# Kernel optimization log

Hardware: AMD Instinct MI355X
Metric: run time of the kernel (lower is better)

Reference implementation:

```python
import jax, jax.numpy as jnp
import numpy as np

B, S, N, P = 16, 1, 6, 70000
H0, W0, DS = 448, 800, 4
H, W = H0 // DS, W0 // DS          # 112, 200
BEV_SIDE = 200


def _apply_4x4(RT, xyz):
    # RT: [M,4,4], xyz: [M,P,3] -> [M,P,3]
    xyz1 = jnp.concatenate([xyz, jnp.ones_like(xyz[..., :1])], axis=-1)
    return jnp.einsum('mij,mpj->mpi', RT, xyz1)[..., :3]


def _scale_intrinsics4(K, sx, sy):
    # K: [M,3,3] pinhole intrinsics -> scaled, embedded in 4x4
    M = K.shape[0]
    K4 = jnp.tile(jnp.eye(4, dtype=K.dtype), (M, 1, 1))
    K4 = K4.at[:, 0, 0].set(K[:, 0, 0] * sx)
    K4 = K4.at[:, 1, 1].set(K[:, 1, 1] * sy)
    K4 = K4.at[:, 0, 2].set(K[:, 0, 2] * sx)
    K4 = K4.at[:, 1, 2].set(K[:, 1, 2] * sy)
    return K4


def setup_inputs() -> dict:
    rng = np.random.default_rng(0)
    pts = rng.uniform(-50.0, 50.0, size=(B, 1, 1, P, 3)).astype(np.float32)
    pts[..., 2] = rng.uniform(-2.0, 4.0, size=(B, 1, 1, P)).astype(np.float32)
    ilu = rng.uniform(0.0, 255.0, size=(B, 1, 1, P, 1)).astype(np.float32)
    pcloud = np.concatenate([pts, ilu], axis=-1)
    # extrinsics: cam-to-car pose, 6 cameras at yaw 0..300deg
    E = np.tile(np.eye(4, dtype=np.float32), (B, S, N, 1, 1))
    for n in range(N):
        a = 2.0 * np.pi * n / N
        c, s = np.cos(a), np.sin(a)
        E[:, :, n, :3, :3] = np.array([[c, -s, 0], [s, c, 0], [0, 0, 1]], np.float32)
        E[:, :, n, :3, 3] = np.array([2.0 * c, 2.0 * s, 1.5], np.float32)
    K = np.tile(np.eye(3, dtype=np.float32), (B, S, N, 1, 1))
    K[..., 0, 0] = 500.0
    K[..., 1, 1] = 500.0
    K[..., 0, 2] = W0 / 2.0
    K[..., 1, 2] = H0 / 2.0
    V = np.tile(np.eye(4, dtype=np.float32), (B, 1, 1, 1, 1))
    V[..., 0, 0] = 2.0
    V[..., 1, 1] = 2.0
    V[..., 0, 3] = 100.0
    V[..., 1, 3] = 100.0
    return {
        'pcloud': jnp.asarray(pcloud),
        'extrinsics': jnp.asarray(E),
        'intrinsics': jnp.asarray(K),
        'view': jnp.asarray(V),
        'bev_side': BEV_SIDE,
    }


def reference(pcloud, extrinsics, intrinsics, view, bev_side):
    sx = sy = 1.0 / DS
    bsn = B * S * N
    lidar_coords = pcloud[:, 0, 0, :, :3]                      # [B,P,3]
    ilu = jnp.repeat(pcloud[:, 0, 0, :, 3], N, axis=0)         # [BSN,P]
    view2 = view[:, 0, 0]                                      # [B,4,4]
    lidar_view = _apply_4x4(jnp.linalg.inv(view2), lidar_coords)
    xyz_car = jnp.repeat(lidar_view, N, axis=0)                # [BSN,P,3]
    K = intrinsics.reshape(bsn, 3, 3)
    E = extrinsics.reshape(bsn, 4, 4)
    Rt = jnp.swapaxes(E[:, :3, :3], 1, 2)
    Einv = E.at[:, :3, :3].set(Rt).at[:, :3, 3:4].set(-jnp.matmul(Rt, E[:, :3, 3:4]))
    pixel_from_car = jnp.matmul(_scale_intrinsics4(K, sx, sy), Einv)
    z = _apply_4x4(Einv, xyz_car)[:, :, 2]                     # cam-frame depth
    xyz_pixel = _apply_4x4(pixel_from_car, xyz_car)            # [BSN,P,3]
    normalizer = xyz_pixel[:, :, 2]
    xy = xyz_pixel[:, :, :2] / jnp.maximum(normalizer[..., None], 1e-6)
    x_, y_ = xy[:, :, 0], xy[:, :, 1]
    valid = ((x_ > -0.5) & (x_ < W - 0.5) & (y_ > -0.5) & (y_ < H - 0.5) & (z > 0.0)).astype(pcloud.dtype)
    depth = jnp.clip(normalizer, 0.0, bev_side / 2 - 1) * valid
    vilu = jnp.clip(ilu * valid, 0.0, 255.0)
    ym = jnp.clip(y_, 0.0, H - 1).astype(jnp.int32)
    xm = jnp.clip(x_, 0.0, W - 1).astype(jnp.int32)
    b = jnp.broadcast_to(jnp.arange(bsn)[:, None], (bsn, P))
    depth_grid = jnp.zeros((bsn, H, W), pcloud.dtype).at[b, ym, xm].set(depth)
    ilu_grid = jnp.zeros((bsn, H, W), pcloud.dtype).at[b, ym, xm].set(vilu)
    ilu_grid = jnp.log1p(ilu_grid) / np.log(256.0)
    depth_grid = depth_grid / (bev_side / 2)
    return jnp.concatenate([depth_grid[:, None], ilu_grid[:, None]], axis=1)  # [BSN,2,H,W]
```

## Files before the change

### kernel.cpp

```cpp
#include <hip/hip_runtime.h>
#include <math.h>

#define B_    16
#define N_    6
#define P_    70000
#define H_    112
#define W_    200
#define HW_   (H_ * W_)
#define BSN_  (B_ * N_)
#define QROWS  28
#define QCELLS (QROWS * W_)
#define THREADS_ 1024

#define WS_NEED ((size_t)BSN_ * P_ * 2)
#define PVEC (P_ / 8)

#define CC0 0u
#define CC1 199u
#define CC2 28416u
#define CC3 28615u


__device__ __forceinline__ float rdot(const float r[4], float x, float y, float z) {
    float s = r[0] * x;
    s = fmaf(r[1], y, s);
    s = fmaf(r[2], z, s);
    return s + r[3];
}

__device__ __forceinline__ float rdot4(float r0, float r1, float r2, float r3,
                                       float x, float y, float z) {
    float s = r0 * x;
    s = fmaf(r1, y, s);
    s = fmaf(r2, z, s);
    return s + r3;
}

__device__ __forceinline__ void inv4(const float* m, float* o) {
    float inv[16];
    inv[0]  =  m[5]*m[10]*m[15] - m[5]*m[11]*m[14] - m[9]*m[6]*m[15] + m[9]*m[7]*m[14] + m[13]*m[6]*m[11] - m[13]*m[7]*m[10];
    inv[4]  = -m[4]*m[10]*m[15] + m[4]*m[11]*m[14] + m[8]*m[6]*m[15] - m[8]*m[7]*m[14] - m[12]*m[6]*m[11] + m[12]*m[7]*m[10];
    inv[8]  =  m[4]*m[9]*m[15]  - m[4]*m[11]*m[13] - m[8]*m[5]*m[15] + m[8]*m[7]*m[13] + m[12]*m[5]*m[11] - m[12]*m[7]*m[9];
    inv[12] = -m[4]*m[9]*m[14]  + m[4]*m[10]*m[13] + m[8]*m[5]*m[14] - m[8]*m[6]*m[13] - m[12]*m[5]*m[10] + m[12]*m[6]*m[9];
    inv[1]  = -m[1]*m[10]*m[15] + m[1]*m[11]*m[14] + m[9]*m[2]*m[15] - m[9]*m[3]*m[14] - m[13]*m[2]*m[11] + m[13]*m[3]*m[10];
    inv[5]  =  m[0]*m[10]*m[15] - m[0]*m[11]*m[14] - m[8]*m[2]*m[15] + m[8]*m[3]*m[14] + m[12]*m[2]*m[11] - m[12]*m[3]*m[10];
    inv[9]  = -m[0]*m[9]*m[15]  + m[0]*m[11]*m[13] + m[8]*m[1]*m[15] - m[8]*m[3]*m[13] - m[12]*m[1]*m[11] + m[12]*m[3]*m[9];
    inv[13] =  m[0]*m[9]*m[14]  - m[0]*m[10]*m[13] - m[8]*m[1]*m[14] + m[8]*m[2]*m[13] + m[12]*m[1]*m[10] - m[12]*m[2]*m[9];
    inv[2]  =  m[1]*m[6]*m[15]  - m[1]*m[7]*m[14]  - m[5]*m[2]*m[15] + m[5]*m[3]*m[14] + m[13]*m[2]*m[7]  - m[13]*m[3]*m[6];
    inv[6]  = -m[0]*m[6]*m[15]  + m[0]*m[7]*m[14]  + m[4]*m[2]*m[15] - m[4]*m[3]*m[14] - m[12]*m[2]*m[7]  + m[12]*m[3]*m[6];
    inv[10] =  m[0]*m[5]*m[15]  - m[0]*m[7]*m[13]  - m[4]*m[1]*m[15] + m[4]*m[3]*m[13] + m[12]*m[1]*m[7]  - m[12]*m[3]*m[5];
    inv[14] = -m[0]*m[5]*m[14]  + m[0]*m[6]*m[13]  + m[4]*m[1]*m[14] - m[4]*m[2]*m[13] - m[12]*m[1]*m[6]  + m[12]*m[2]*m[5];
    inv[3]  = -m[1]*m[6]*m[11]  + m[1]*m[7]*m[10]  + m[5]*m[2]*m[11] - m[5]*m[3]*m[10] - m[9]*m[2]*m[7]   + m[9]*m[3]*m[6];
    inv[7]  =  m[0]*m[6]*m[11]  - m[0]*m[7]*m[10]  - m[4]*m[2]*m[11] + m[4]*m[3]*m[10] + m[8]*m[2]*m[7]   - m[8]*m[3]*m[6];
    inv[11] = -m[0]*m[5]*m[11]  + m[0]*m[7]*m[9]   + m[4]*m[1]*m[11] - m[4]*m[3]*m[9]  - m[8]*m[1]*m[7]   + m[8]*m[3]*m[5];
    inv[15] =  m[0]*m[5]*m[10]  - m[0]*m[6]*m[9]   - m[4]*m[1]*m[10] + m[4]*m[2]*m[9]  + m[8]*m[1]*m[6]   - m[8]*m[2]*m[5];
    float det = m[0]*inv[0] + m[1]*inv[4] + m[2]*inv[8] + m[3]*inv[12];
    float rdet = 1.0f / det;
    for (int i = 0; i < 16; ++i) o[i] = inv[i] * rdet;
}

__device__ __forceinline__ void cam_mats(const float* Ein, const float* Kin,
                                         float E2[4], float PFC[3][4]) {
    float Einv[4][4];
    for (int i = 0; i < 3; ++i)
        for (int j = 0; j < 3; ++j)
            Einv[i][j] = Ein[j * 4 + i];
    for (int i = 0; i < 3; ++i) {
        float s = Ein[0 * 4 + i] * Ein[0 * 4 + 3];
        s = fmaf(Ein[1 * 4 + i], Ein[1 * 4 + 3], s);
        s = fmaf(Ein[2 * 4 + i], Ein[2 * 4 + 3], s);
        Einv[i][3] = -s;
    }
    Einv[3][0] = Ein[12]; Einv[3][1] = Ein[13];
    Einv[3][2] = Ein[14]; Einv[3][3] = Ein[15];

    float K4[4][4] = {};
    K4[0][0] = Kin[0] * 0.25f;  K4[0][2] = Kin[2] * 0.25f;
    K4[1][1] = Kin[4] * 0.25f;  K4[1][2] = Kin[5] * 0.25f;
    K4[2][2] = 1.0f;            K4[3][3] = 1.0f;

    for (int i = 0; i < 3; ++i)
        for (int j = 0; j < 4; ++j) {
            float s = K4[i][0] * Einv[0][j];
            s = fmaf(K4[i][1], Einv[1][j], s);
            s = fmaf(K4[i][2], Einv[2][j], s);
            s = fmaf(K4[i][3], Einv[3][j], s);
            PFC[i][j] = s;
        }
    for (int j = 0; j < 4; ++j) E2[j] = Einv[2][j];
}


#define K1T 256

__global__ __launch_bounds__(K1T) void k_codes(
        const float4* __restrict__ pc, const float* __restrict__ extr,
        const float* __restrict__ intr, const float* __restrict__ view,
        unsigned short* __restrict__ codes) {
    __shared__ float sM[84];
    const int b = blockIdx.x;
    const int t = threadIdx.x;
    if (t == 0) {
        float Vi[16];
        inv4(&view[b * 16], Vi);
        for (int k = 0; k < 12; ++k) sM[k] = Vi[k];
    } else if (t >= 64 && t < 64 + N_) {
        int n = t - 64;
        float E2[4], PFC[3][4];
        cam_mats(&extr[(b * N_ + n) * 16], &intr[(b * N_ + n) * 9], E2, PFC);
        for (int i = 0; i < 3; ++i)
            for (int j = 0; j < 4; ++j) sM[12 + n * 12 + i * 4 + j] = PFC[i][j];
    }
    __syncthreads();

    const int p = blockIdx.y * K1T + t;
    if (p >= P_) return;
    float4 pt = pc[(size_t)b * P_ + p];
    float lx = rdot(&sM[0], pt.x, pt.y, pt.z);
    float ly = rdot(&sM[4], pt.x, pt.y, pt.z);
    float lz = rdot(&sM[8], pt.x, pt.y, pt.z);
    #pragma unroll
    for (int n = 0; n < 6; ++n) {
        const float* Pm = &sM[12 + n * 12];
        float px = rdot(&Pm[0], lx, ly, lz);
        float py = rdot(&Pm[4], lx, ly, lz);
        float pz = rdot(&Pm[8], lx, ly, lz);
        float denom = fmaxf(pz, 1e-6f);
        float x_ = px / denom;
        float y_ = py / denom;
        int ym = (int)fminf(fmaxf(y_, 0.0f), (float)(H_ - 1));
        int xm = (int)fminf(fmaxf(x_, 0.0f), (float)(W_ - 1));
        codes[(size_t)(b * N_ + n) * P_ + p] = (unsigned short)((ym << 8) | xm);
    }
}


__global__ __launch_bounds__(THREADS_) void k_scatfin(
        const float4* __restrict__ pc, const unsigned short* __restrict__ codes,
        const float* __restrict__ extr, const float* __restrict__ intr,
        const float* __restrict__ view,
        float* __restrict__ out, const int* __restrict__ bev_side_p) {
    __shared__ int   win[QCELLS];
    __shared__ float sM[28];

    const int i   = blockIdx.x;
    const int xcd = i & 7;
    const int j   = i >> 3;
    const int b   = xcd + 8 * (j >= 24 ? 1 : 0);
    const int r   = j % 24;
    const int cam = r >> 2;
    const int q   = r & 3;
    const int m   = b * N_ + cam;
    const int rlo = q * QROWS;
    const int t   = threadIdx.x;

    if (t == 0) {
        float Vi[16];
        inv4(&view[b * 16], Vi);
        for (int k = 0; k < 12; ++k) sM[k] = Vi[k];
    } else if (t == 64) {
        float E2[4], PFC[3][4];
        cam_mats(&extr[m * 16], &intr[m * 9], E2, PFC);
        for (int ii = 0; ii < 3; ++ii)
            for (int jj = 0; jj < 4; ++jj) sM[12 + ii * 4 + jj] = PFC[ii][jj];
        for (int jj = 0; jj < 4; ++jj) sM[24 + jj] = E2[jj];
    }
    for (int k = t; k < QCELLS; k += THREADS_) win[k] = -1;
    __syncthreads();

    const uint4* cm4 = (const uint4*)(codes + (size_t)m * P_);
    int c0 = -1, c1 = -1, c2 = -1, c3 = -1;
    for (int v = t; v < PVEC; v += THREADS_) {
        uint4 w4 = cm4[v];
        int pbase = v * 8;
        unsigned int cs[4] = {w4.x, w4.y, w4.z, w4.w};
        #pragma unroll
        for (int h = 0; h < 4; ++h) {
            #pragma unroll
            for (int lohi = 0; lohi < 2; ++lohi) {
                unsigned int c = lohi ? (cs[h] >> 16) : (cs[h] & 0xffffu);
                int p = pbase + h * 2 + lohi;
                bool i0 = (c == CC0), i1 = (c == CC1),
                     i2 = (c == CC2), i3 = (c == CC3);
                c0 = i0 ? p : c0;  c1 = i1 ? p : c1;
                c2 = i2 ? p : c2;  c3 = i3 ? p : c3;
                int rr = (int)(c >> 8) - rlo;
                if (!(i0 | i1 | i2 | i3) && (unsigned)rr < (unsigned)QROWS)
                    atomicMax(&win[rr * W_ + (int)(c & 255u)], p);
            }
        }
    }
    for (int d = 32; d; d >>= 1) {
        c0 = max(c0, __shfl_xor(c0, d));
        c1 = max(c1, __shfl_xor(c1, d));
        c2 = max(c2, __shfl_xor(c2, d));
        c3 = max(c3, __shfl_xor(c3, d));
    }
    if ((t & 63) == 0) {
        if (q == 0) {
            if (c0 >= 0) atomicMax(&win[0],   c0);
            if (c1 >= 0) atomicMax(&win[199], c1);
        } else if (q == 3) {
            if (c2 >= 0) atomicMax(&win[(H_ - 1 - rlo) * W_ + 0],   c2);
            if (c3 >= 0) atomicMax(&win[(H_ - 1 - rlo) * W_ + 199], c3);
        }
    }
    __syncthreads();

    const float bev_half = (float)bev_side_p[0] * 0.5f;
    const float clip_hi  = bev_half - 1.0f;
    const float4* pcb = pc + (size_t)b * P_;
    const int base0 = (m * 2) * HW_ + rlo * W_;
    for (int rr = t; rr < QCELLS; rr += THREADS_) {
        int w = win[rr];
        float depth = 0.0f, iluv = 0.0f;
        if (w >= 0) {
            float4 pt = pcb[w];
            float lx = rdot4(sM[0],  sM[1],  sM[2],  sM[3],  pt.x, pt.y, pt.z);
            float ly = rdot4(sM[4],  sM[5],  sM[6],  sM[7],  pt.x, pt.y, pt.z);
            float lz = rdot4(sM[8],  sM[9],  sM[10], sM[11], pt.x, pt.y, pt.z);
            float z  = rdot4(sM[24], sM[25], sM[26], sM[27], lx, ly, lz);
            float px = rdot4(sM[12], sM[13], sM[14], sM[15], lx, ly, lz);
            float py = rdot4(sM[16], sM[17], sM[18], sM[19], lx, ly, lz);
            float pz = rdot4(sM[20], sM[21], sM[22], sM[23], lx, ly, lz);
            float denom = fmaxf(pz, 1e-6f);
            float x_ = px / denom;
            float y_ = py / denom;
            bool valid = (x_ > -0.5f) && (x_ < (float)W_ - 0.5f) &&
                         (y_ > -0.5f) && (y_ < (float)H_ - 0.5f) && (z > 0.0f);
            if (valid) {
                float d = fminf(fmaxf(pz, 0.0f), clip_hi);
                depth = d / bev_half;
                float vi = fminf(fmaxf(pt.w, 0.0f), 255.0f);
                iluv = log1pf(vi) / 5.545177444479562f;
            }
        }
        out[base0 + rr]       = depth;
        out[base0 + HW_ + rr] = iluv;
    }
}


#define HALF_ 56
#define CELLS_ (HALF_ * W_)

__global__ __launch_bounds__(THREADS_) void k_lidar_fused(
        const float4* __restrict__ pc, const float* __restrict__ extr,
        const float* __restrict__ intr, const float* __restrict__ view,
        float* __restrict__ out, const int* __restrict__ bev_side_p) {
    __shared__ int   win[CELLS_];
    __shared__ float sV[4][4];
    __shared__ float sE2[4];
    __shared__ float sP[3][4];

    const int i    = blockIdx.x;
    const int xcd  = i & 7;
    const int s    = i >> 3;
    const int b    = xcd + 8 * (s >= 12 ? 1 : 0);
    const int c12  = s % 12;
    const int m    = b * N_ + (c12 >> 1);
    const int rlo  = (c12 & 1) * HALF_;
    const int t    = threadIdx.x;

    if (t == 0) {
        float Vi[16];
        inv4(&view[b * 16], Vi);
        for (int ii = 0; ii < 4; ++ii)
            for (int jj = 0; jj < 4; ++jj) sV[ii][jj] = Vi[ii * 4 + jj];
    } else if (t == 64) {
        float E2[4], PFC[3][4];
        cam_mats(&extr[m * 16], &intr[m * 9], E2, PFC);
        for (int jj = 0; jj < 4; ++jj) sE2[jj] = E2[jj];
        for (int ii = 0; ii < 3; ++ii)
            for (int jj = 0; jj < 4; ++jj) sP[ii][jj] = PFC[ii][jj];
    }
    for (int k = t; k < CELLS_; k += THREADS_) win[k] = -1;
    __syncthreads();

    const float4* pcb = pc + (size_t)b * P_;
    int c0 = -1, c1 = -1, c2 = -1, c3 = -1;
    for (int p = t; p < P_; p += THREADS_) {
        float4 pt = pcb[p];
        float lx = rdot(sV[0], pt.x, pt.y, pt.z);
        float ly = rdot(sV[1], pt.x, pt.y, pt.z);
        float lz = rdot(sV[2], pt.x, pt.y, pt.z);
        float px = rdot(sP[0], lx, ly, lz);
        float py = rdot(sP[1], lx, ly, lz);
        float pz = rdot(sP[2], lx, ly, lz);
        float denom = fmaxf(pz, 1e-6f);
        float x_ = px / denom;
        float y_ = py / denom;
        int ym = (int)fminf(fmaxf(y_, 0.0f), (float)(H_ - 1));
        int xm = (int)fminf(fmaxf(x_, 0.0f), (float)(W_ - 1));
        bool is_c = (xm == 0 || xm == W_ - 1) && (ym == 0 || ym == H_ - 1);
        int code = ((ym != 0) << 1) | (xm != 0);
        c0 = (is_c && code == 0) ? p : c0;
        c1 = (is_c && code == 1) ? p : c1;
        c2 = (is_c && code == 2) ? p : c2;
        c3 = (is_c && code == 3) ? p : c3;
        int rr = ym - rlo;
        if (!is_c && (unsigned)rr < (unsigned)HALF_)
            atomicMax(&win[rr * W_ + xm], p);
    }
    for (int d = 32; d; d >>= 1) {
        c0 = max(c0, __shfl_xor(c0, d));
        c1 = max(c1, __shfl_xor(c1, d));
        c2 = max(c2, __shfl_xor(c2, d));
        c3 = max(c3, __shfl_xor(c3, d));
    }
    if ((t & 63) == 0) {
        if (rlo == 0) {
            if (c0 >= 0) atomicMax(&win[0],   c0);
            if (c1 >= 0) atomicMax(&win[199], c1);
        } else {
            if (c2 >= 0) atomicMax(&win[(H_ - 1 - rlo) * W_ + 0],   c2);
            if (c3 >= 0) atomicMax(&win[(H_ - 1 - rlo) * W_ + 199], c3);
        }
    }
    __syncthreads();

    const float bev_half = (float)bev_side_p[0] * 0.5f;
    const float clip_hi  = bev_half - 1.0f;
    const int base0 = (m * 2) * HW_ + rlo * W_;
    for (int rr = t; rr < CELLS_; rr += THREADS_) {
        int w = win[rr];
        float depth = 0.0f, iluv = 0.0f;
        if (w >= 0) {
            float4 pt = pcb[w];
            float lx = rdot(sV[0], pt.x, pt.y, pt.z);
            float ly = rdot(sV[1], pt.x, pt.y, pt.z);
            float lz = rdot(sV[2], pt.x, pt.y, pt.z);
            float z  = rdot(sE2,   lx, ly, lz);
            float px = rdot(sP[0], lx, ly, lz);
            float py = rdot(sP[1], lx, ly, lz);
            float pz = rdot(sP[2], lx, ly, lz);
            float denom = fmaxf(pz, 1e-6f);
            float x_ = px / denom;
            float y_ = py / denom;
            bool valid = (x_ > -0.5f) && (x_ < (float)W_ - 0.5f) &&
                         (y_ > -0.5f) && (y_ < (float)H_ - 0.5f) && (z > 0.0f);
            if (valid) {
                float d = fminf(fmaxf(pz, 0.0f), clip_hi);
                depth = d / bev_half;
                float vi = fminf(fmaxf(pt.w, 0.0f), 255.0f);
                iluv = log1pf(vi) / 5.545177444479562f;
            }
        }
        out[base0 + rr]       = depth;
        out[base0 + HW_ + rr] = iluv;
    }
}


extern "C" void kernel_launch(void* const* d_in, const int* in_sizes, int n_in,
                              void* d_out, int out_size, void* d_ws, size_t ws_size,
                              hipStream_t stream) {
    const float4* pc  = (const float4*)d_in[0];
    const float* extr = (const float*)d_in[1];
    const float* intr = (const float*)d_in[2];
    const float* view = (const float*)d_in[3];
    const int*   bev  = (const int*)d_in[4];
    float* out = (float*)d_out;

    if (ws_size >= WS_NEED) {
        unsigned short* codes = (unsigned short*)d_ws;
        k_codes<<<dim3(B_, (P_ + K1T - 1) / K1T), dim3(K1T), 0, stream>>>(
            pc, extr, intr, view, codes);
        k_scatfin<<<dim3(BSN_ * 4), dim3(THREADS_), 0, stream>>>(
            pc, codes, extr, intr, view, out, bev);
    } else {
        k_lidar_fused<<<dim3(BSN_ * 2), dim3(THREADS_), 0, stream>>>(
            pc, extr, intr, view, out, bev);
    }
}
```

Before: 48.15 us.

## Bucket projected points by row slab so scatter blocks read only their own slab

The first kernel now sorts each point's projected cell code into per-camera, per-row-quarter buckets. It uses wave ballots, per-wave counts and a global atomic cursor, and packs code and point index into one 32-bit word. The scatter kernel then reads only the entries that belong to its quarter, instead of scanning all 70k codes for every quarter, which cuts redundant reads and compare work roughly fourfold. In exchange it adds an extra cursor-init launch and global atomics, and writes a larger 32-bit arena instead of 16-bit codes. Ordering inside a bucket is nondeterministic, but the atomicMax on the point index keeps last-write-wins semantics.

```diff
diff --git a/kernel.cpp b/kernel.cpp
--- a/kernel.cpp
+++ b/kernel.cpp
@@ -10,15 +10,12 @@
 #define BSN_  (B_ * N_)
 #define QROWS  28
 #define QCELLS (QROWS * W_)
+#define NSLAB  4
 #define THREADS_ 1024
 
-#define WS_NEED ((size_t)BSN_ * P_ * 2)
-#define PVEC (P_ / 8)
-
-#define CC0 0u
-#define CC1 199u
-#define CC2 28416u
-#define CC3 28615u
+#define NBUCKET (BSN_ * NSLAB)
+#define ARENA_U32 ((size_t)NBUCKET * P_)
+#define WS_NEED ((ARENA_U32 + NBUCKET) * 4)
 
 
 __device__ __forceinline__ float rdot(const float r[4], float x, float y, float z) {
@@ -91,15 +88,27 @@
 }
 
 
-#define K1T 256
-
-__global__ __launch_bounds__(K1T) void k_codes(
+__global__ __launch_bounds__(NBUCKET) void k_init_cursors(int* __restrict__ cursors) {
+    cursors[threadIdx.x] = 0;
+}
+
+
+#define K1CH 69
+
+__global__ __launch_bounds__(THREADS_) void k_bucket(
         const float4* __restrict__ pc, const float* __restrict__ extr,
         const float* __restrict__ intr, const float* __restrict__ view,
-        unsigned short* __restrict__ codes) {
+        unsigned int* __restrict__ arena, int* __restrict__ cursors) {
     __shared__ float sM[84];
-    const int b = blockIdx.x;
-    const int t = threadIdx.x;
+    __shared__ int   cnt[16][24];
+    __shared__ int   wbase[16][24];
+    __shared__ int   gb[24];
+
+    const int b    = blockIdx.x;
+    const int t    = threadIdx.x;
+    const int lane = t & 63;
+    const int w    = t >> 6;
+
     if (t == 0) {
         float Vi[16];
         inv4(&view[b * 16], Vi);
@@ -113,12 +122,17 @@
     }
     __syncthreads();
 
-    const int p = blockIdx.y * K1T + t;
-    if (p >= P_) return;
-    float4 pt = pc[(size_t)b * P_ + p];
+    const int p = blockIdx.y * THREADS_ + t;
+    const bool valid = (p < P_);
+    float4 pt = make_float4(0.f, 0.f, 0.f, 0.f);
+    if (valid) pt = pc[(size_t)b * P_ + p];
     float lx = rdot(&sM[0], pt.x, pt.y, pt.z);
     float ly = rdot(&sM[4], pt.x, pt.y, pt.z);
     float lz = rdot(&sM[8], pt.x, pt.y, pt.z);
+
+    const unsigned long long lt = (1ull << lane) - 1ull;
+    int stash[6];
+
     #pragma unroll
     for (int n = 0; n < 6; ++n) {
         const float* Pm = &sM[12 + n * 12];
@@ -130,13 +144,49 @@
         float y_ = py / denom;
         int ym = (int)fminf(fmaxf(y_, 0.0f), (float)(H_ - 1));
         int xm = (int)fminf(fmaxf(x_, 0.0f), (float)(W_ - 1));
-        codes[(size_t)(b * N_ + n) * P_ + p] = (unsigned short)((ym << 8) | xm);
-    }
-}
-
-
-__global__ __launch_bounds__(THREADS_) void k_scatfin(
-        const float4* __restrict__ pc, const unsigned short* __restrict__ codes,
+        int code = (ym << 8) | xm;
+        int slab = (ym * 585) >> 14;
+        unsigned long long ACT = __ballot(valid);
+        unsigned long long B0  = __ballot(valid && (slab & 1));
+        unsigned long long B1  = __ballot(valid && (slab & 2));
+        unsigned long long m   = ((slab & 1) ? B0 : ~B0) &
+                                 ((slab & 2) ? B1 : ~B1) & ACT;
+        int rank = (int)__popcll(m & lt);
+        if (lane < 4) {
+            unsigned long long ml = ((lane & 1) ? B0 : ~B0) &
+                                    ((lane & 2) ? B1 : ~B1) & ACT;
+            cnt[w][n * 4 + lane] = (int)__popcll(ml);
+        }
+        stash[n] = (code << 9) | (rank << 3) | slab;
+    }
+    __syncthreads();
+
+    if (t < 24) {
+        int s = 0;
+        for (int w2 = 0; w2 < 16; ++w2) { wbase[w2][t] = s; s += cnt[w2][t]; }
+        gb[t] = atomicAdd(&cursors[b * 24 + t], s);
+    }
+    __syncthreads();
+
+    if (valid) {
+        #pragma unroll
+        for (int n = 0; n < 6; ++n) {
+            int sv   = stash[n];
+            int slab = sv & 7;
+            int rank = (sv >> 3) & 63;
+            int code = sv >> 9;
+            int j    = n * 4 + slab;
+            size_t slot = (size_t)((b * N_ + n) * NSLAB + slab) * P_ +
+                          (size_t)(gb[j] + wbase[w][j] + rank);
+            arena[slot] = ((unsigned int)code << 17) | (unsigned int)p;
+        }
+    }
+}
+
+
+__global__ __launch_bounds__(THREADS_) void k_scatfin2(
+        const float4* __restrict__ pc, const unsigned int* __restrict__ arena,
+        const int* __restrict__ cursors,
         const float* __restrict__ extr, const float* __restrict__ intr,
         const float* __restrict__ view,
         float* __restrict__ out, const int* __restrict__ bev_side_p) {
@@ -168,41 +218,55 @@
     for (int k = t; k < QCELLS; k += THREADS_) win[k] = -1;
     __syncthreads();
 
-    const uint4* cm4 = (const uint4*)(codes + (size_t)m * P_);
-    int c0 = -1, c1 = -1, c2 = -1, c3 = -1;
-    for (int v = t; v < PVEC; v += THREADS_) {
-        uint4 w4 = cm4[v];
-        int pbase = v * 8;
-        unsigned int cs[4] = {w4.x, w4.y, w4.z, w4.w};
+    const unsigned int* seg = arena + (size_t)(m * NSLAB + q) * P_;
+    const int cntq = cursors[b * 24 + cam * 4 + q];
+    const int ccA = (q == 0) ? 0   : ((q == 3) ? ((111 << 8) | 0)   : -1);
+    const int ccB = (q == 0) ? 199 : ((q == 3) ? ((111 << 8) | 199) : -1);
+    int cA = -1, cB = -1;
+
+    const int nv = cntq >> 2;
+    const uint4* seg4 = (const uint4*)seg;
+    for (int v = t; v < nv; v += THREADS_) {
+        uint4 e4 = seg4[v];
+        unsigned int es[4] = {e4.x, e4.y, e4.z, e4.w};
         #pragma unroll
         for (int h = 0; h < 4; ++h) {
-            #pragma unroll
-            for (int lohi = 0; lohi < 2; ++lohi) {
-                unsigned int c = lohi ? (cs[h] >> 16) : (cs[h] & 0xffffu);
-                int p = pbase + h * 2 + lohi;
-                bool i0 = (c == CC0), i1 = (c == CC1),
-                     i2 = (c == CC2), i3 = (c == CC3);
-                c0 = i0 ? p : c0;  c1 = i1 ? p : c1;
-                c2 = i2 ? p : c2;  c3 = i3 ? p : c3;
-                int rr = (int)(c >> 8) - rlo;
-                if (!(i0 | i1 | i2 | i3) && (unsigned)rr < (unsigned)QROWS)
-                    atomicMax(&win[rr * W_ + (int)(c & 255u)], p);
+            unsigned int e = es[h];
+            int code = (int)(e >> 17);
+            int p    = (int)(e & 0x1FFFFu);
+            if (code == ccA)      cA = max(cA, p);
+            else if (code == ccB) cB = max(cB, p);
+            else {
+                int ym = code >> 8, xm = code & 255;
+                atomicMax(&win[(ym - rlo) * W_ + xm], p);
             }
         }
     }
+    {
+        int k2 = (nv << 2) + t;
+        if (k2 < cntq) {
+            unsigned int e = seg[k2];
+            int code = (int)(e >> 17);
+            int p    = (int)(e & 0x1FFFFu);
+            if (code == ccA)      cA = max(cA, p);
+            else if (code == ccB) cB = max(cB, p);
+            else {
+                int ym = code >> 8, xm = code & 255;
+                atomicMax(&win[(ym - rlo) * W_ + xm], p);
+            }
+        }
+    }
     for (int d = 32; d; d >>= 1) {
-        c0 = max(c0, __shfl_xor(c0, d));
-        c1 = max(c1, __shfl_xor(c1, d));
-        c2 = max(c2, __shfl_xor(c2, d));
-        c3 = max(c3, __shfl_xor(c3, d));
+        cA = max(cA, __shfl_xor(cA, d));
+        cB = max(cB, __shfl_xor(cB, d));
     }
     if ((t & 63) == 0) {
         if (q == 0) {
-            if (c0 >= 0) atomicMax(&win[0],   c0);
-            if (c1 >= 0) atomicMax(&win[199], c1);
+            if (cA >= 0) atomicMax(&win[0],   cA);
+            if (cB >= 0) atomicMax(&win[199], cB);
         } else if (q == 3) {
-            if (c2 >= 0) atomicMax(&win[(H_ - 1 - rlo) * W_ + 0],   c2);
-            if (c3 >= 0) atomicMax(&win[(H_ - 1 - rlo) * W_ + 199], c3);
+            if (cA >= 0) atomicMax(&win[(H_ - 1 - rlo) * W_ + 0],   cA);
+            if (cB >= 0) atomicMax(&win[(H_ - 1 - rlo) * W_ + 199], cB);
         }
     }
     __syncthreads();
@@ -212,10 +276,10 @@
     const float4* pcb = pc + (size_t)b * P_;
     const int base0 = (m * 2) * HW_ + rlo * W_;
     for (int rr = t; rr < QCELLS; rr += THREADS_) {
-        int w = win[rr];
+        int wv = win[rr];
         float depth = 0.0f, iluv = 0.0f;
-        if (w >= 0) {
-            float4 pt = pcb[w];
+        if (wv >= 0) {
+            float4 pt = pcb[wv];
             float lx = rdot4(sM[0],  sM[1],  sM[2],  sM[3],  pt.x, pt.y, pt.z);
             float ly = rdot4(sM[4],  sM[5],  sM[6],  sM[7],  pt.x, pt.y, pt.z);
             float lz = rdot4(sM[8],  sM[9],  sM[10], sM[11], pt.x, pt.y, pt.z);
@@ -363,11 +427,13 @@
     float* out = (float*)d_out;
 
     if (ws_size >= WS_NEED) {
-        unsigned short* codes = (unsigned short*)d_ws;
-        k_codes<<<dim3(B_, (P_ + K1T - 1) / K1T), dim3(K1T), 0, stream>>>(
-            pc, extr, intr, view, codes);
-        k_scatfin<<<dim3(BSN_ * 4), dim3(THREADS_), 0, stream>>>(
-            pc, codes, extr, intr, view, out, bev);
+        unsigned int* arena = (unsigned int*)d_ws;
+        int* cursors = (int*)(arena + ARENA_U32);
+        k_init_cursors<<<dim3(1), dim3(NBUCKET), 0, stream>>>(cursors);
+        k_bucket<<<dim3(B_, K1CH), dim3(THREADS_), 0, stream>>>(
+            pc, extr, intr, view, arena, cursors);
+        k_scatfin2<<<dim3(NBUCKET), dim3(THREADS_), 0, stream>>>(
+            pc, arena, cursors, extr, intr, view, out, bev);
     } else {
         k_lidar_fused<<<dim3(BSN_ * 2), dim3(THREADS_), 0, stream>>>(
             pc, extr, intr, view, out, bev);
```

Measured after the change: 56.06 us. 1.16x slower.
